# Performance work log

Hardware: AMD Instinct MI355X
Metric: run time of the kernel (lower is better)

## Reference

```python
import jax, jax.numpy as jnp
import numpy as np

H = 512          # lstm_hidden_size
NUM_OPS = 8
NUM_NODES = 4
TEMP = 5.0
TANH_C = 2.5
B = 4096
NUM_STEPS = 16   # 8 lstm steps x 2 decisions (node, op)


def setup_inputs() -> dict:
    key = jax.random.key(0)
    ks = jax.random.split(key, 20)
    u = lambda k, s: jax.random.uniform(k, s, jnp.float32, -0.1, 0.1)
    inp = {}
    # embedding: torch default init N(0,1)
    inp["emb"] = jax.random.normal(ks[0], (NUM_OPS + 1, H), jnp.float32)
    # LSTM (single layer), torch gate order i,f,g,o; init U(-0.1,0.1), bias 0
    inp["w_ih"] = u(ks[1], (4 * H, H))
    inp["w_hh"] = u(ks[2], (4 * H, H))
    inp["b_ih"] = jnp.zeros((4 * H,), jnp.float32)
    inp["b_hh"] = jnp.zeros((4 * H,), jnp.float32)
    # node-predecessor decoders: widths 2,3,4,5 (one per intermediate node)
    inp["wn2"] = u(ks[3], (2, H)); inp["bn2"] = jnp.zeros((2,), jnp.float32)
    inp["wn3"] = u(ks[4], (3, H)); inp["bn3"] = jnp.zeros((3,), jnp.float32)
    inp["wn4"] = u(ks[5], (4, H)); inp["bn4"] = jnp.zeros((4,), jnp.float32)
    inp["wn5"] = u(ks[6], (5, H)); inp["bn5"] = jnp.zeros((5,), jnp.float32)
    # op decoders: one [NUM_OPS, H] decoder per intermediate node
    inp["wop"] = u(ks[7], (NUM_NODES, NUM_OPS, H))
    inp["bop"] = jnp.zeros((NUM_NODES, NUM_OPS), jnp.float32)
    # Gumbel noise for multinomial sampling via Gumbel-max (padded to width 8)
    un = jax.random.uniform(ks[8], (NUM_STEPS, B, NUM_OPS), jnp.float32,
                            minval=1e-6, maxval=1.0 - 1e-6)
    inp["gumbel"] = -jnp.log(-jnp.log(un))
    inp["batch_size"] = B
    return inp


def _lstm_step(x, h, c, w_ih, w_hh, b_ih, b_hh):
    gates = x @ w_ih.T + h @ w_hh.T + b_ih + b_hh   # [B, 4H]
    i, f, g, o = jnp.split(gates, 4, axis=-1)
    i = jax.nn.sigmoid(i); f = jax.nn.sigmoid(f)
    g = jnp.tanh(g);       o = jax.nn.sigmoid(o)
    c = f * c + i * g
    h = o * jnp.tanh(c)
    return h, c


def _decide(logits, g):
    # logits: [B, k], g: [B, k] gumbel noise -> sample ~ softmax(logits)
    logp = jax.nn.log_softmax(logits, axis=-1)
    probs = jnp.exp(logp)
    action = jnp.argmax(logits + g, axis=-1)                     # [B]
    sel = jnp.take_along_axis(logp, action[:, None], 1)[:, 0]     # [B]
    ent = -(logp * probs).sum(-1)                                 # [B]
    return action, sel, ent


def reference(emb, w_ih, w_hh, b_ih, b_hh,
              wn2, bn2, wn3, bn3, wn4, bn4, wn5, bn5,
              wop, bop, gumbel, batch_size):
    node_dec = [(wn2, bn2), (wn3, bn3), (wn4, bn4), (wn5, bn5)]
    h = jnp.zeros((batch_size, H), emb.dtype)
    c = jnp.zeros((batch_size, H), emb.dtype)
    inputs = jnp.zeros((batch_size,), jnp.int32)   # initial token 0
    actions, log_probs, entropies = [], [], []
    step = 0
    for i in range(NUM_NODES):
        wn, bn = node_dec[i]
        k = wn.shape[0]
        for _ in range(2):  # two (prev_node, op) edges per node, one lstm step each
            x = emb[inputs]                                   # [B, H]
            h, c = _lstm_step(x, h, c, w_ih, w_hh, b_ih, b_hh)
            # node-predecessor decision: temperature + tanh squashing
            nl = TANH_C * jnp.tanh((h @ wn.T + bn) / TEMP)    # [B, k]
            a, s, e = _decide(nl, gumbel[step, :, :k])
            actions.append(a); log_probs.append(s); entropies.append(e)
            step += 1
            # op decision: temperature only (no tanh in original code)
            ol = (h @ wop[i].T + bop[i]) / TEMP               # [B, NUM_OPS]
            a, s, e = _decide(ol, gumbel[step])
            actions.append(a); log_probs.append(s); entropies.append(e)
            step += 1
            inputs = a  # op action feeds the next lstm step
    return (jnp.stack(actions).astype(jnp.int32),   # [16, B]
            jnp.stack(log_probs),                   # [16, B]
            jnp.stack(entropies))                   # [16, B]
```

## Files before the change

### kernel.cpp

```cpp
#include <hip/hip_runtime.h>


constexpr int Bsz = 4096;
constexpr int Hsz = 512;
constexpr int G4H = 2048;

typedef unsigned short ushort_t;
using short8 = __attribute__((ext_vector_type(8))) short;
using f32x4 = __attribute__((ext_vector_type(4))) float;

__device__ __forceinline__ ushort_t f2bf_hi(float f) {
  unsigned u = __float_as_uint(f);
  u += 0x7FFF + ((u >> 16) & 1);
  return (ushort_t)(u >> 16);
}
__device__ __forceinline__ float bf2f(ushort_t h) {
  return __uint_as_float((unsigned)h << 16);
}

__device__ __forceinline__ void glds16(const void* gsrc, void* ldst) {
  __builtin_amdgcn_global_load_lds(
      (const __attribute__((address_space(1))) void*)gsrc,
      (__attribute__((address_space(3))) void*)ldst, 16, 0, 0);
}

__global__ __launch_bounds__(256) void precompute_E(
    const float* __restrict__ emb, const float* __restrict__ w_ih,
    const float* __restrict__ b_ih, const float* __restrict__ b_hh,
    float* __restrict__ E, float* __restrict__ Eperm) {
  int idx = blockIdx.x * 256 + threadIdx.x;
  int t = idx >> 11;
  int col = idx & 2047;
  const float* er = emb + (size_t)t * Hsz;
  const float* wr = w_ih + (size_t)col * Hsz;
  float acc = 0.0f;
  for (int k = 0; k < Hsz; k += 4) {
    float4 e = *(const float4*)(er + k);
    float4 w = *(const float4*)(wr + k);
    acc += e.x * w.x + e.y * w.y + e.z * w.z + e.w * w.w;
  }
  float v = acc + b_ih[col] + b_hh[col];
  E[idx] = v;
  int g = col >> 9, j = col & 511;
  Eperm[(size_t)t * G4H + (j << 2) + g] = v;
}

__global__ __launch_bounds__(256) void build_wcat(
    const float* __restrict__ w_hh, ushort_t* __restrict__ Wcat) {
  int ct = blockIdx.y;
  int k = blockIdx.x * 256 + threadIdx.x;
  int j = ct >> 2, g = ct & 3;
  const float* srcrow = w_hh + (size_t)(g * 512 + j) * Hsz;
  ushort_t out;
  if (k < 512) {
    out = f2bf_hi(srcrow[k]);
  } else if (k < 1024) {
    float x = srcrow[k - 512];
    ushort_t hi = f2bf_hi(x);
    out = f2bf_hi(x - bf2f(hi));
  } else {
    out = f2bf_hi(srcrow[k - 1024]);
  }
  Wcat[(size_t)ct * 1536 + k] = out;
}

__global__ __launch_bounds__(256) void class_gemm(
    const float* __restrict__ h, const float* __restrict__ w,
    float* __restrict__ G, int nq) {
  const int wid = (blockIdx.x << 2) + (threadIdx.x >> 6);
  const int lane = threadIdx.x & 63;
  const int q = wid >> 11;
  const int col = wid & 2047;
  if (q >= nq) return;
  const float* hr = h + (size_t)q * Hsz + (lane << 3);
  const float* wr = w + (size_t)col * Hsz + (lane << 3);
  float4 a0 = *(const float4*)(hr);
  float4 a1 = *(const float4*)(hr + 4);
  float4 b0 = *(const float4*)(wr);
  float4 b1 = *(const float4*)(wr + 4);
  float v = a0.x * b0.x + a0.y * b0.y + a0.z * b0.z + a0.w * b0.w +
            a1.x * b1.x + a1.y * b1.y + a1.z * b1.z + a1.w * b1.w;
#pragma unroll
  for (int off = 32; off > 0; off >>= 1) v += __shfl_xor(v, off, 64);
  if (lane == 0) G[(size_t)q * G4H + col] = v;
}

__global__ __launch_bounds__(256) void gemm64(
    const float* __restrict__ A, const float* __restrict__ Bw,
    float* __restrict__ G) {
  constexpr int LDA = 68;
  __shared__ float As[16 * LDA];
  __shared__ float Bs[16 * LDA];
  const int tid = threadIdx.x;
  const int bx = blockIdx.x & 31;
  const int by = blockIdx.x >> 5;
  const int r0 = by * 64, c0 = bx * 64;
  const int tx = tid & 15, ty = tid >> 4;
  const int lr = tid >> 2;
  const int lk = (tid & 3) << 2;
  const float* Ar = A + (size_t)(r0 + lr) * Hsz;
  const float* Br = Bw + (size_t)(c0 + lr) * Hsz;
  float acc[4][4];
#pragma unroll
  for (int i = 0; i < 4; ++i)
#pragma unroll
    for (int j = 0; j < 4; ++j) acc[i][j] = 0.0f;

  for (int k0 = 0; k0 < Hsz; k0 += 16) {
    float4 a = *(const float4*)(Ar + k0 + lk);
    float4 b = *(const float4*)(Br + k0 + lk);
    __syncthreads();
    As[(lk + 0) * LDA + lr] = a.x;
    As[(lk + 1) * LDA + lr] = a.y;
    As[(lk + 2) * LDA + lr] = a.z;
    As[(lk + 3) * LDA + lr] = a.w;
    Bs[(lk + 0) * LDA + lr] = b.x;
    Bs[(lk + 1) * LDA + lr] = b.y;
    Bs[(lk + 2) * LDA + lr] = b.z;
    Bs[(lk + 3) * LDA + lr] = b.w;
    __syncthreads();
#pragma unroll
    for (int kk = 0; kk < 16; ++kk) {
      float4 av = *(const float4*)&As[kk * LDA + (ty << 2)];
      float4 bv = *(const float4*)&Bs[kk * LDA + (tx << 2)];
      float avs[4] = {av.x, av.y, av.z, av.w};
      float bvs[4] = {bv.x, bv.y, bv.z, bv.w};
#pragma unroll
      for (int i = 0; i < 4; ++i)
#pragma unroll
        for (int j = 0; j < 4; ++j) acc[i][j] = fmaf(avs[i], bvs[j], acc[i][j]);
    }
  }
#pragma unroll
  for (int i = 0; i < 4; ++i)
#pragma unroll
    for (int j = 0; j < 4; ++j)
      G[(size_t)(r0 + (ty << 2) + i) * G4H + c0 + (tx << 2) + j] = acc[i][j];
}

__global__ __launch_bounds__(256) void step_pw(
    const float* __restrict__ G, const float* __restrict__ E,
    const float* __restrict__ c_prev, float* __restrict__ h_out,
    float* __restrict__ c_out, int nq) {
  int idx = blockIdx.x * 256 + threadIdx.x;
  if (idx >= nq * Hsz) return;
  int q = idx >> 9, j = idx & 511;
  int gq = q >> 3, er = q & 7;
  const float* Eg = E + (size_t)er * G4H;
  float iv = Eg[j], fv = Eg[512 + j], gv = Eg[1024 + j], ov = Eg[1536 + j];
  if (G) {
    const float* Gg = G + (size_t)gq * G4H;
    iv += Gg[j]; fv += Gg[512 + j]; gv += Gg[1024 + j]; ov += Gg[1536 + j];
  }
  float cp = c_prev ? c_prev[(size_t)gq * Hsz + j] : 0.0f;
  float ig = 1.0f / (1.0f + expf(-iv));
  float fg = 1.0f / (1.0f + expf(-fv));
  float gg = tanhf(gv);
  float og = 1.0f / (1.0f + expf(-ov));
  float cn = fg * cp + ig * gg;
  c_out[idx] = cn;
  h_out[idx] = og * tanhf(cn);
}

__global__ __launch_bounds__(256) void expand_pw(
    const float* __restrict__ G, const float* __restrict__ E,
    const float* __restrict__ c4, const int* __restrict__ cls3,
    const int* __restrict__ act3, float* __restrict__ h_out,
    float* __restrict__ c_out, ushort_t* __restrict__ Acat) {
  int idx = blockIdx.x * 256 + threadIdx.x;
  int r = idx >> 9, j = idx & 511;
  int q = cls3[r], er = act3[r];
  const float* Eg = E + (size_t)er * G4H;
  const float* Gg = G + (size_t)q * G4H;
  float iv = Gg[j] + Eg[j];
  float fv = Gg[512 + j] + Eg[512 + j];
  float gv = Gg[1024 + j] + Eg[1024 + j];
  float ov = Gg[1536 + j] + Eg[1536 + j];
  float cp = c4[(size_t)q * Hsz + j];
  float ig = 1.0f / (1.0f + expf(-iv));
  float fg = 1.0f / (1.0f + expf(-fv));
  float gg = tanhf(gv);
  float og = 1.0f / (1.0f + expf(-ov));
  float cn = fg * cp + ig * gg;
  float hn = og * tanhf(cn);
  c_out[idx] = cn;
  h_out[idx] = hn;
  ushort_t hi = f2bf_hi(hn);
  Acat[(size_t)r * 1024 + j] = hi;
  Acat[(size_t)r * 1024 + 512 + j] = f2bf_hi(hn - bf2f(hi));
}

__global__ __launch_bounds__(256) void gemm_bf16_lstm(
    const ushort_t* __restrict__ Acat, const ushort_t* __restrict__ Wcat,
    const float* __restrict__ Eperm, const int* __restrict__ act,
    float* __restrict__ cF, float* __restrict__ h_out,
    ushort_t* __restrict__ Aout) {
  __shared__ union {
    struct { ushort_t A[128 * 64]; ushort_t B[128 * 64]; } s[2];
    float C[64 * 132];
  } sm;

  const int tid = threadIdx.x;
  const int wave = tid >> 6, lane = tid & 63;
  const int xcd = blockIdx.x & 7;
  const int i64 = blockIdx.x >> 3;
  const int by = ((xcd >> 1) << 3) + (i64 >> 3);
  const int bx = ((xcd & 1) << 3) + (i64 & 7);
  const int r0 = by * 128, c0 = bx * 128;
  const int wr = (wave >> 1) * 64, wc = (wave & 1) * 64;
  const int mrow = lane & 15, quad = lane >> 4;

  const int slr = lane >> 3;
  const int ssw = ((lane & 7) ^ slr) << 3;

  f32x4 acc[4][4];
#pragma unroll
  for (int i = 0; i < 4; ++i)
#pragma unroll
    for (int jt = 0; jt < 4; ++jt) acc[i][jt] = (f32x4){0.f, 0.f, 0.f, 0.f};

  auto stage = [&](int buf, int k0) {
    const int ak = (k0 < 512) ? k0 : k0 - 512;
#pragma unroll
    for (int q = 0; q < 8; ++q) {
      const int g = (q << 2) + wave;
      if (g < 16) {
        const int row = r0 + g * 8 + slr;
        glds16(Acat + (size_t)row * 1024 + ak + ssw,
               (char*)sm.s[buf].A + g * 1024);
      } else {
        const int row = c0 + (g - 16) * 8 + slr;
        glds16(Wcat + (size_t)row * 1536 + k0 + ssw,
               (char*)sm.s[buf].B + (g - 16) * 1024);
      }
    }
  };

  stage(0, 0);
  __syncthreads();

  int cur = 0;
  for (int it = 0; it < 24; ++it) {
    if (it < 23) stage(cur ^ 1, (it + 1) << 6);
    const ushort_t* As = sm.s[cur].A;
    const ushort_t* Bs = sm.s[cur].B;
#pragma unroll
    for (int kk = 0; kk < 2; ++kk) {
      const int swr = ((kk * 4 + quad) ^ (mrow & 7)) << 3;
      short8 a[4], b[4];
#pragma unroll
      for (int i = 0; i < 4; ++i)
        a[i] = *(const short8*)&As[(wr + i * 16 + mrow) * 64 + swr];
#pragma unroll
      for (int jt = 0; jt < 4; ++jt)
        b[jt] = *(const short8*)&Bs[(wc + jt * 16 + mrow) * 64 + swr];
#pragma unroll
      for (int i = 0; i < 4; ++i)
#pragma unroll
        for (int jt = 0; jt < 4; ++jt)
          acc[i][jt] = __builtin_amdgcn_mfma_f32_16x16x32_bf16(
              a[i], b[jt], acc[i][jt], 0, 0, 0);
    }
    __syncthreads();
    cur ^= 1;
  }

  const int jj = tid & 31;
  const int rbase = tid >> 5;
#pragma unroll
  for (int p = 0; p < 2; ++p) {
    __syncthreads();
    if ((wr >> 6) == p) {
#pragma unroll
      for (int i = 0; i < 4; ++i)
#pragma unroll
        for (int jt = 0; jt < 4; ++jt)
#pragma unroll
          for (int rg = 0; rg < 4; ++rg)
            sm.C[(i * 16 + quad * 4 + rg) * 132 + wc + jt * 16 + mrow] =
                acc[i][jt][rg];
    }
    __syncthreads();
#pragma unroll
    for (int rp = 0; rp < 8; ++rp) {
      const int rl = rbase * 8 + rp;
      const int grow = r0 + p * 64 + rl;
      float4 g4 = *(float4*)&sm.C[rl * 132 + jj * 4];
      const int a = act[grow];
      const int jglob = (c0 >> 2) + jj;
      float4 e4 = *(const float4*)&Eperm[(size_t)a * G4H + c0 + jj * 4];
      float iv = g4.x + e4.x, fv = g4.y + e4.y;
      float gv = g4.z + e4.z, ov = g4.w + e4.w;
      float ig = 1.0f / (1.0f + expf(-iv));
      float fg = 1.0f / (1.0f + expf(-fv));
      float gg = tanhf(gv);
      float og = 1.0f / (1.0f + expf(-ov));
      const size_t ci = (size_t)grow * Hsz + jglob;
      float cn = fg * cF[ci] + ig * gg;
      float hn = og * tanhf(cn);
      cF[ci] = cn;
      h_out[ci] = hn;
      ushort_t hi = f2bf_hi(hn);
      Aout[(size_t)grow * 1024 + jglob] = hi;
      Aout[(size_t)grow * 1024 + 512 + jglob] = f2bf_hi(hn - bf2f(hi));
    }
  }
}

template <int K>
__global__ __launch_bounds__(256) void decide_step(
    const float* __restrict__ h, const float* __restrict__ wn,
    const float* __restrict__ bn, const float* __restrict__ wopi,
    const float* __restrict__ bopi, const float* __restrict__ gum,
    float* __restrict__ oan, float* __restrict__ oao,
    float* __restrict__ oln, float* __restrict__ olo,
    float* __restrict__ oen, float* __restrict__ oeo,
    int* __restrict__ act_next, const int* __restrict__ hidx, int hmode,
    const int* __restrict__ cls_prev, int* __restrict__ cls_out) {
  const int lane = threadIdx.x & 63;
  const int r = (blockIdx.x << 2) + (threadIdx.x >> 6);
  const int idx = (hmode == 0) ? 0 : (hmode == 1 ? r : hidx[r]);
  const float* hr = h + (size_t)idx * Hsz;
  const float4 hv0 = *(const float4*)(hr + (lane << 3));
  const float4 hv1 = *(const float4*)(hr + (lane << 3) + 4);

  float nl[K];
#pragma unroll
  for (int j = 0; j < K; ++j) {
    const float* w = wn + (size_t)j * Hsz;
    float4 w0 = *(const float4*)(w + (lane << 3));
    float4 w1 = *(const float4*)(w + (lane << 3) + 4);
    float v = hv0.x * w0.x + hv0.y * w0.y + hv0.z * w0.z + hv0.w * w0.w +
              hv1.x * w1.x + hv1.y * w1.y + hv1.z * w1.z + hv1.w * w1.w;
#pragma unroll
    for (int off = 32; off > 0; off >>= 1) v += __shfl_xor(v, off, 64);
    nl[j] = 2.5f * tanhf((v + bn[j]) / 5.0f);
  }
  float ol[8];
#pragma unroll
  for (int j = 0; j < 8; ++j) {
    const float* w = wopi + (size_t)j * Hsz;
    float4 w0 = *(const float4*)(w + (lane << 3));
    float4 w1 = *(const float4*)(w + (lane << 3) + 4);
    float v = hv0.x * w0.x + hv0.y * w0.y + hv0.z * w0.z + hv0.w * w0.w +
              hv1.x * w1.x + hv1.y * w1.y + hv1.z * w1.z + hv1.w * w1.w;
#pragma unroll
    for (int off = 32; off > 0; off >>= 1) v += __shfl_xor(v, off, 64);
    ol[j] = (v + bopi[j]) / 5.0f;
  }

  {
    const float* g = gum + (size_t)r * 8;
    float m = nl[0];
#pragma unroll
    for (int j = 1; j < K; ++j) m = fmaxf(m, nl[j]);
    float se = 0.0f;
#pragma unroll
    for (int j = 0; j < K; ++j) se += expf(nl[j] - m);
    float lse = logf(se);
    int a = 0;
    float best = nl[0] + g[0];
#pragma unroll
    for (int j = 1; j < K; ++j) {
      float v = nl[j] + g[j];
      if (v > best) { best = v; a = j; }
    }
    float ent = 0.0f, sel = 0.0f;
#pragma unroll
    for (int j = 0; j < K; ++j) {
      float lp = nl[j] - m - lse;
      ent -= lp * expf(lp);
      if (j == a) sel = lp;
    }
    if (lane == 0) { oan[r] = (float)a; oln[r] = sel; oen[r] = ent; }
  }
  {
    const float* g = gum + (size_t)Bsz * 8 + (size_t)r * 8;
    float m = ol[0];
#pragma unroll
    for (int j = 1; j < 8; ++j) m = fmaxf(m, ol[j]);
    float se = 0.0f;
#pragma unroll
    for (int j = 0; j < 8; ++j) se += expf(ol[j] - m);
    float lse = logf(se);
    int a = 0;
    float best = ol[0] + g[0];
#pragma unroll
    for (int j = 1; j < 8; ++j) {
      float v = ol[j] + g[j];
      if (v > best) { best = v; a = j; }
    }
    float ent = 0.0f, sel = 0.0f;
#pragma unroll
    for (int j = 0; j < 8; ++j) {
      float lp = ol[j] - m - lse;
      ent -= lp * expf(lp);
      if (j == a) sel = lp;
    }
    if (lane == 0) {
      oao[r] = (float)a; olo[r] = sel; oeo[r] = ent;
      act_next[r] = a;
      if (cls_out) cls_out[r] = (cls_prev ? cls_prev[r] * 8 : 0) + a;
    }
  }
}

extern "C" void kernel_launch(void* const* d_in, const int* in_sizes, int n_in,
                              void* d_out, int out_size, void* d_ws,
                              size_t ws_size, hipStream_t stream) {
  (void)in_sizes; (void)n_in; (void)out_size; (void)ws_size;
  const float* emb = (const float*)d_in[0];
  const float* w_ih = (const float*)d_in[1];
  const float* w_hh = (const float*)d_in[2];
  const float* b_ih = (const float*)d_in[3];
  const float* b_hh = (const float*)d_in[4];
  const float* wn[4] = {(const float*)d_in[5], (const float*)d_in[7],
                        (const float*)d_in[9], (const float*)d_in[11]};
  const float* bn[4] = {(const float*)d_in[6], (const float*)d_in[8],
                        (const float*)d_in[10], (const float*)d_in[12]};
  const float* wop = (const float*)d_in[13];
  const float* bop = (const float*)d_in[14];
  const float* gum = (const float*)d_in[15];

  float* ws = (float*)d_ws;
  float* E = ws;                 ws += 9 * G4H;
  float* Eperm = ws;             ws += 9 * G4H;
  float* h1 = ws;                ws += Hsz;
  float* c1 = ws;                ws += Hsz;
  float* h2 = ws;                ws += 8 * Hsz;
  float* c2 = ws;                ws += 8 * Hsz;
  float* h3 = ws;                ws += 64 * Hsz;
  float* c3 = ws;                ws += 64 * Hsz;
  float* h4 = ws;                ws += 512 * Hsz;
  float* c4 = ws;                ws += 512 * Hsz;
  float* Gearly = ws;
  ushort_t* AcatB = (ushort_t*)Gearly;
  ws += (8u << 20) / 4;
  ushort_t* AcatA = (ushort_t*)ws;      ws += (8u << 20) / 4;
  ushort_t* Wcat = (ushort_t*)ws;       ws += (6u << 20) / 4;
  float* hA = ws;                ws += (size_t)Bsz * Hsz;
  float* cF = ws;                ws += (size_t)Bsz * Hsz;
  int* act = (int*)ws;
  int* cls = act + Bsz;

  float* out = (float*)d_out;
  const size_t SZ = (size_t)16 * Bsz;

  auto decide = [&](int s, const float* h, int hmode, const int* hidx,
                    const int* cls_prev, int* cls_out) {
    const int i = s >> 1;
    float* oan = out + (size_t)(2 * s) * Bsz;
    float* oao = out + (size_t)(2 * s + 1) * Bsz;
    float* oln = out + SZ + (size_t)(2 * s) * Bsz;
    float* olo = out + SZ + (size_t)(2 * s + 1) * Bsz;
    float* oen = out + 2 * SZ + (size_t)(2 * s) * Bsz;
    float* oeo = out + 2 * SZ + (size_t)(2 * s + 1) * Bsz;
    const float* gn = gum + (size_t)(2 * s) * Bsz * 8;
    const float* wopi = wop + (size_t)i * 8 * Hsz;
    const float* bopi = bop + (size_t)i * 8;
    switch (i) {
      case 0:
        decide_step<2><<<Bsz / 4, 256, 0, stream>>>(h, wn[0], bn[0], wopi, bopi,
            gn, oan, oao, oln, olo, oen, oeo, act, hidx, hmode, cls_prev, cls_out);
        break;
      case 1:
        decide_step<3><<<Bsz / 4, 256, 0, stream>>>(h, wn[1], bn[1], wopi, bopi,
            gn, oan, oao, oln, olo, oen, oeo, act, hidx, hmode, cls_prev, cls_out);
        break;
      case 2:
        decide_step<4><<<Bsz / 4, 256, 0, stream>>>(h, wn[2], bn[2], wopi, bopi,
            gn, oan, oao, oln, olo, oen, oeo, act, hidx, hmode, cls_prev, cls_out);
        break;
      default:
        decide_step<5><<<Bsz / 4, 256, 0, stream>>>(h, wn[3], bn[3], wopi, bopi,
            gn, oan, oao, oln, olo, oen, oeo, act, hidx, hmode, cls_prev, cls_out);
        break;
    }
  };

  precompute_E<<<(9 * G4H) / 256, 256, 0, stream>>>(emb, w_ih, b_ih, b_hh, E,
                                                    Eperm);
  build_wcat<<<dim3(6, 2048), 256, 0, stream>>>(w_hh, Wcat);

  step_pw<<<2, 256, 0, stream>>>(nullptr, E, nullptr, h1, c1, 1);
  decide(0, h1, 0, nullptr, nullptr, cls);

  class_gemm<<<512, 256, 0, stream>>>(h1, w_hh, Gearly, 1);
  step_pw<<<16, 256, 0, stream>>>(Gearly, E, c1, h2, c2, 8);
  decide(1, h2, 2, cls, cls, cls);

  class_gemm<<<4096, 256, 0, stream>>>(h2, w_hh, Gearly, 8);
  step_pw<<<128, 256, 0, stream>>>(Gearly, E, c2, h3, c3, 64);
  decide(2, h3, 2, cls, cls, cls);

  class_gemm<<<32768, 256, 0, stream>>>(h3, w_hh, Gearly, 64);
  step_pw<<<1024, 256, 0, stream>>>(Gearly, E, c3, h4, c4, 512);
  decide(3, h4, 2, cls, nullptr, nullptr);

  gemm64<<<256, 256, 0, stream>>>(h4, w_hh, Gearly);
  expand_pw<<<(Bsz * Hsz) / 256, 256, 0, stream>>>(Gearly, E, c4, cls, act, hA,
                                                   cF, AcatA);
  decide(4, hA, 1, nullptr, nullptr, nullptr);

  ushort_t* ain = AcatA;
  ushort_t* aout = AcatB;
  for (int s = 5; s < 8; ++s) {
    gemm_bf16_lstm<<<512, 256, 0, stream>>>(ain, Wcat, Eperm, act, cF, hA, aout);
    decide(s, hA, 1, nullptr, nullptr, nullptr);
    ushort_t* t = ain; ain = aout; aout = t;
  }
}
```

Baseline: 417.6 us.

## Restructure split-bf16 LSTM GEMM into hi/lo panels sharing one A/B fetch

The recurrent GEMM used to stream A as [hi,lo,hi] against W as [hi,lo,hi] over K=1536. It now loads the hi and lo panels of both A and W for each 32-wide K slice and issues three MFMAs (hh, hl, lh). That cuts global traffic and loop iterations from 24 to 16, and Wcat shrinks to 1024 columns. precompute_E now reduces each dot product across a wave with shuffles instead of one thread per output, and the early class GEMM for 64 classes is swapped to gemm64. The new LDS layout drops the XOR swizzle, so LDS bank conflicts may increase.

```diff
diff --git a/kernel.cpp b/kernel.cpp
--- a/kernel.cpp
+++ b/kernel.cpp
@@ -28,21 +28,26 @@
     const float* __restrict__ emb, const float* __restrict__ w_ih,
     const float* __restrict__ b_ih, const float* __restrict__ b_hh,
     float* __restrict__ E, float* __restrict__ Eperm) {
-  int idx = blockIdx.x * 256 + threadIdx.x;
-  int t = idx >> 11;
-  int col = idx & 2047;
-  const float* er = emb + (size_t)t * Hsz;
-  const float* wr = w_ih + (size_t)col * Hsz;
-  float acc = 0.0f;
-  for (int k = 0; k < Hsz; k += 4) {
-    float4 e = *(const float4*)(er + k);
-    float4 w = *(const float4*)(wr + k);
-    acc += e.x * w.x + e.y * w.y + e.z * w.z + e.w * w.w;
-  }
-  float v = acc + b_ih[col] + b_hh[col];
-  E[idx] = v;
-  int g = col >> 9, j = col & 511;
-  Eperm[(size_t)t * G4H + (j << 2) + g] = v;
+  const int lane = threadIdx.x & 63;
+  const int wid = (blockIdx.x << 2) + (threadIdx.x >> 6);
+  const int t = wid >> 11;
+  const int col = wid & 2047;
+  const float* er = emb + (size_t)t * Hsz + (lane << 3);
+  const float* wr = w_ih + (size_t)col * Hsz + (lane << 3);
+  float4 e0 = *(const float4*)(er);
+  float4 e1 = *(const float4*)(er + 4);
+  float4 w0 = *(const float4*)(wr);
+  float4 w1 = *(const float4*)(wr + 4);
+  float v = e0.x * w0.x + e0.y * w0.y + e0.z * w0.z + e0.w * w0.w +
+            e1.x * w1.x + e1.y * w1.y + e1.z * w1.z + e1.w * w1.w;
+#pragma unroll
+  for (int off = 32; off > 0; off >>= 1) v += __shfl_xor(v, off, 64);
+  if (lane == 0) {
+    float val = v + b_ih[col] + b_hh[col];
+    E[wid] = val;
+    int g = col >> 9, j = col & 511;
+    Eperm[(size_t)t * G4H + (j << 2) + g] = val;
+  }
 }
 
 __global__ __launch_bounds__(256) void build_wcat(
@@ -54,12 +59,10 @@
   ushort_t out;
   if (k < 512) {
     out = f2bf_hi(srcrow[k]);
-  } else if (k < 1024) {
+  } else {
     float x = srcrow[k - 512];
     ushort_t hi = f2bf_hi(x);
     out = f2bf_hi(x - bf2f(hi));
-  } else {
-    out = f2bf_hi(srcrow[k - 1024]);
   }
   Wcat[(size_t)ct * 1536 + k] = out;
 }
@@ -196,7 +199,7 @@
     float* __restrict__ cF, float* __restrict__ h_out,
     ushort_t* __restrict__ Aout) {
   __shared__ union {
-    struct { ushort_t A[128 * 64]; ushort_t B[128 * 64]; } s[2];
+    ushort_t P[2][4][128 * 32];
     float C[64 * 132];
   } sm;
 
@@ -210,8 +213,27 @@
   const int wr = (wave >> 1) * 64, wc = (wave & 1) * 64;
   const int mrow = lane & 15, quad = lane >> 4;
 
-  const int slr = lane >> 3;
-  const int ssw = ((lane & 7) ^ slr) << 3;
+  const int srow = lane >> 2;
+  const int sk = (lane & 3) << 3;
+
+  const ushort_t* sbase[8];
+  int doff[8];
+#pragma unroll
+  for (int q = 0; q < 8; ++q) {
+    const int g = (q << 2) + wave;
+    const int panel = g >> 3;
+    const int region = g & 7;
+    const int row = region * 16 + srow;
+    if (panel == 0)
+      sbase[q] = Acat + (size_t)(r0 + row) * 1024 + sk;
+    else if (panel == 1)
+      sbase[q] = Acat + (size_t)(r0 + row) * 1024 + 512 + sk;
+    else if (panel == 2)
+      sbase[q] = Wcat + (size_t)(c0 + row) * 1536 + sk;
+    else
+      sbase[q] = Wcat + (size_t)(c0 + row) * 1536 + 512 + sk;
+    doff[q] = panel * 8192 + region * 1024;
+  }
 
   f32x4 acc[4][4];
 #pragma unroll
@@ -219,48 +241,45 @@
 #pragma unroll
     for (int jt = 0; jt < 4; ++jt) acc[i][jt] = (f32x4){0.f, 0.f, 0.f, 0.f};
 
-  auto stage = [&](int buf, int k0) {
-    const int ak = (k0 < 512) ? k0 : k0 - 512;
-#pragma unroll
-    for (int q = 0; q < 8; ++q) {
-      const int g = (q << 2) + wave;
-      if (g < 16) {
-        const int row = r0 + g * 8 + slr;
-        glds16(Acat + (size_t)row * 1024 + ak + ssw,
-               (char*)sm.s[buf].A + g * 1024);
-      } else {
-        const int row = c0 + (g - 16) * 8 + slr;
-        glds16(Wcat + (size_t)row * 1536 + k0 + ssw,
-               (char*)sm.s[buf].B + (g - 16) * 1024);
-      }
-    }
+  auto stage = [&](int buf, int it) {
+    const int ks = it << 5;
+#pragma unroll
+    for (int q = 0; q < 8; ++q)
+      glds16(sbase[q] + ks, (char*)sm.P[0][0] + (buf << 15) + doff[q]);
   };
 
   stage(0, 0);
   __syncthreads();
 
   int cur = 0;
-  for (int it = 0; it < 24; ++it) {
-    if (it < 23) stage(cur ^ 1, (it + 1) << 6);
-    const ushort_t* As = sm.s[cur].A;
-    const ushort_t* Bs = sm.s[cur].B;
-#pragma unroll
-    for (int kk = 0; kk < 2; ++kk) {
-      const int swr = ((kk * 4 + quad) ^ (mrow & 7)) << 3;
-      short8 a[4], b[4];
-#pragma unroll
-      for (int i = 0; i < 4; ++i)
-        a[i] = *(const short8*)&As[(wr + i * 16 + mrow) * 64 + swr];
-#pragma unroll
-      for (int jt = 0; jt < 4; ++jt)
-        b[jt] = *(const short8*)&Bs[(wc + jt * 16 + mrow) * 64 + swr];
-#pragma unroll
-      for (int i = 0; i < 4; ++i)
-#pragma unroll
-        for (int jt = 0; jt < 4; ++jt)
-          acc[i][jt] = __builtin_amdgcn_mfma_f32_16x16x32_bf16(
-              a[i], b[jt], acc[i][jt], 0, 0, 0);
-    }
+  for (int it = 0; it < 16; ++it) {
+    if (it < 15) stage(cur ^ 1, it + 1);
+    const ushort_t* AH = sm.P[cur][0];
+    const ushort_t* AL = sm.P[cur][1];
+    const ushort_t* BH = sm.P[cur][2];
+    const ushort_t* BL = sm.P[cur][3];
+    short8 ah[4], al[4], bh[4], bl[4];
+#pragma unroll
+    for (int i = 0; i < 4; ++i) {
+      ah[i] = *(const short8*)&AH[(wr + i * 16 + mrow) * 32 + (quad << 3)];
+      al[i] = *(const short8*)&AL[(wr + i * 16 + mrow) * 32 + (quad << 3)];
+    }
+#pragma unroll
+    for (int jt = 0; jt < 4; ++jt) {
+      bh[jt] = *(const short8*)&BH[(wc + jt * 16 + mrow) * 32 + (quad << 3)];
+      bl[jt] = *(const short8*)&BL[(wc + jt * 16 + mrow) * 32 + (quad << 3)];
+    }
+#pragma unroll
+    for (int i = 0; i < 4; ++i)
+#pragma unroll
+      for (int jt = 0; jt < 4; ++jt) {
+        acc[i][jt] = __builtin_amdgcn_mfma_f32_16x16x32_bf16(
+            ah[i], bh[jt], acc[i][jt], 0, 0, 0);
+        acc[i][jt] = __builtin_amdgcn_mfma_f32_16x16x32_bf16(
+            ah[i], bl[jt], acc[i][jt], 0, 0, 0);
+        acc[i][jt] = __builtin_amdgcn_mfma_f32_16x16x32_bf16(
+            al[i], bh[jt], acc[i][jt], 0, 0, 0);
+      }
     __syncthreads();
     cur ^= 1;
   }
@@ -478,9 +497,9 @@
     }
   };
 
-  precompute_E<<<(9 * G4H) / 256, 256, 0, stream>>>(emb, w_ih, b_ih, b_hh, E,
-                                                    Eperm);
-  build_wcat<<<dim3(6, 2048), 256, 0, stream>>>(w_hh, Wcat);
+  precompute_E<<<(9 * G4H) / 4, 256, 0, stream>>>(emb, w_ih, b_ih, b_hh, E,
+                                                  Eperm);
+  build_wcat<<<dim3(4, 2048), 256, 0, stream>>>(w_hh, Wcat);
 
   step_pw<<<2, 256, 0, stream>>>(nullptr, E, nullptr, h1, c1, 1);
   decide(0, h1, 0, nullptr, nullptr, cls);
@@ -493,7 +512,7 @@
   step_pw<<<128, 256, 0, stream>>>(Gearly, E, c2, h3, c3, 64);
   decide(2, h3, 2, cls, cls, cls);
 
-  class_gemm<<<32768, 256, 0, stream>>>(h3, w_hh, Gearly, 64);
+  gemm64<<<32, 256, 0, stream>>>(h3, w_hh, Gearly);
   step_pw<<<1024, 256, 0, stream>>>(Gearly, E, c3, h4, c4, 512);
   decide(3, h4, 2, cls, nullptr, nullptr);
 
```

New measurement: 395.0 us. 5.4% less time.
